# Kernel tuning notes

Hardware: AMD Instinct MI355X
Metric: run time of the kernel (lower is better)

Reference implementation:

```python
import jax, jax.numpy as jnp
import numpy as np

MAX_H = 64
MAX_W = 64

def setup_inputs() -> dict:
    key = jax.random.key(0)
    ks = jax.random.split(key, 6)
    in_f, out_f = 128, 128
    x0 = jax.random.normal(ks[0], (32, 64, 64, in_f), dtype=jnp.float32)
    x1 = jax.random.normal(ks[1], (32, 32, 64, in_f), dtype=jnp.float32)
    x2 = jax.random.normal(ks[2], (32, 64, 32, in_f), dtype=jnp.float32)
    x3 = jax.random.normal(ks[3], (32, 32, 32, in_f), dtype=jnp.float32)
    stdv = 1.0 / np.sqrt(in_f)
    weight = jax.random.uniform(ks[4], (out_f, in_f), minval=-stdv, maxval=stdv, dtype=jnp.float32)
    bias = jax.random.uniform(ks[5], (out_f,), minval=-stdv, maxval=stdv, dtype=jnp.float32)
    return {"x0": x0, "x1": x1, "x2": x2, "x3": x3, "weight": weight, "bias": bias}

def reference(x0, x1, x2, x3, weight, bias):
    # Grouped/ragged linear: flatten each variable-shaped tensor to rows of
    # in_features, concatenate, apply shared y = x @ W^T + b, then reshape to
    # (-1, max_H, max_W, out_features) as in the original CUDA path.
    k = weight.shape[0]
    flat = jnp.concatenate([x.reshape(-1, x.shape[-1]) for x in (x0, x1, x2, x3)], axis=0)
    out = flat @ weight.T + bias  # [total_rows, out_features]
    return out.reshape(-1, MAX_H, MAX_W, k)
```

## Files before the change

kernel.cpp:

```cpp
#include <hip/hip_runtime.h>
#include <hip/hip_bf16.h>


typedef __attribute__((ext_vector_type(8))) short bf8_t;
typedef __attribute__((ext_vector_type(4))) float f4_t;

__device__ __forceinline__ short bfc(float f) {
    return __builtin_bit_cast(short, __float2bfloat16(f));
}

__device__ __forceinline__ unsigned short f2bf_rne(float f) {
    unsigned u = __builtin_bit_cast(unsigned, f);
    u += 0x7fffu + ((u >> 16) & 1u);
    return (unsigned short)(u >> 16);
}

#define SEG0 131072L
#define SEG1 196608L
#define SEG2 262144L

__device__ __forceinline__ void resolve(long gr,
    const float* __restrict__ x0, const float* __restrict__ x1,
    const float* __restrict__ x2, const float* __restrict__ x3,
    float* __restrict__ out, const float** xr, float** orow)
{
    const float* xp; long loc;
    if      (gr < SEG0) { xp = x0; loc = gr; }
    else if (gr < SEG1) { xp = x1; loc = gr - SEG0; }
    else if (gr < SEG2) { xp = x2; loc = gr - SEG1; }
    else                { xp = x3; loc = gr - SEG2; }
    *xr   = xp + loc * 128;
    *orow = out + gr * 128;
}

__device__ __forceinline__ void load_tile(f4_t (&raw)[8], const float* __restrict__ rowbase, int lk)
{
#pragma unroll
    for (int ks = 0; ks < 4; ++ks) {
        const float* p = rowbase + ks * 32 + lk * 8;
        raw[2 * ks]     = *reinterpret_cast<const f4_t*>(p);
        raw[2 * ks + 1] = *reinterpret_cast<const f4_t*>(p + 4);
    }
}

__device__ __forceinline__ void compute_store(
    const f4_t (&raw)[8], const unsigned short* __restrict__ Wl,
    const float* __restrict__ bl, float* __restrict__ orow,
    int lm, int lk, int nsw)
{
    bf8_t xf[4];
#pragma unroll
    for (int ks = 0; ks < 4; ++ks) {
        bf8_t t;
        t[0] = bfc(raw[2 * ks].x);
        t[1] = bfc(raw[2 * ks].y);
        t[2] = bfc(raw[2 * ks].z);
        t[3] = bfc(raw[2 * ks].w);
        t[4] = bfc(raw[2 * ks + 1].x);
        t[5] = bfc(raw[2 * ks + 1].y);
        t[6] = bfc(raw[2 * ks + 1].z);
        t[7] = bfc(raw[2 * ks + 1].w);
        xf[ks] = t;
    }

    f4_t acc[8];
#pragma unroll
    for (int nt = 0; nt < 8; ++nt)
        acc[nt] = *reinterpret_cast<const f4_t*>(&bl[nt * 16 + lk * 4]);

#pragma unroll
    for (int nt = 0; nt < 8; ++nt) {
        const int nrow = nt * 16 + lm;
#pragma unroll
        for (int ks = 0; ks < 4; ++ks) {
            const int c = (ks * 4 + lk) ^ nsw;
            bf8_t wf = *reinterpret_cast<const bf8_t*>(&Wl[nrow * 128 + c * 8]);
            acc[nt] = __builtin_amdgcn_mfma_f32_16x16x32_bf16(wf, xf[ks], acc[nt], 0, 0, 0);
        }
    }

#pragma unroll
    for (int nt = 0; nt < 8; ++nt)
        __builtin_nontemporal_store(acc[nt], reinterpret_cast<f4_t*>(orow + nt * 16 + lk * 4));
}

__global__ __launch_bounds__(256)
void lin_kernel(const float* __restrict__ x0, const float* __restrict__ x1,
                const float* __restrict__ x2, const float* __restrict__ x3,
                const float* __restrict__ W, const float* __restrict__ bias,
                float* __restrict__ out)
{
    __shared__ unsigned short Wl[128 * 128];
    __shared__ float bl[128];

    const int tid = threadIdx.x;

#pragma unroll
    for (int i = 0; i < 16; ++i) {
        int f  = i * 256 + tid;
        int n  = f >> 5;
        int k4 = f & 31;
        f4_t v = reinterpret_cast<const f4_t*>(W)[f];
        unsigned long long p =
              (unsigned long long)f2bf_rne(v.x)
            | ((unsigned long long)f2bf_rne(v.y) << 16)
            | ((unsigned long long)f2bf_rne(v.z) << 32)
            | ((unsigned long long)f2bf_rne(v.w) << 48);
        int sc = (k4 >> 1) ^ (n & 7);
        *reinterpret_cast<unsigned long long*>(&Wl[n * 128 + sc * 8 + (k4 & 1) * 4]) = p;
    }
    if (tid < 128) bl[tid] = bias[tid];
    __syncthreads();

    const int wave = tid >> 6;
    const int lane = tid & 63;
    const int lm   = lane & 15;
    const int lk   = lane >> 4;
    const int nsw  = lm & 7;

    const long r0 = (long)blockIdx.x * 384 + wave * 96 + lm;

    f4_t rawA[8], rawB[8];
    const float* xA; const float* xB;
    float* oA; float* oB;

    resolve(r0 +  0, x0, x1, x2, x3, out, &xA, &oA); load_tile(rawA, xA, lk);
    resolve(r0 + 16, x0, x1, x2, x3, out, &xB, &oB); load_tile(rawB, xB, lk);
    compute_store(rawA, Wl, bl, oA, lm, lk, nsw);
    resolve(r0 + 32, x0, x1, x2, x3, out, &xA, &oA); load_tile(rawA, xA, lk);
    compute_store(rawB, Wl, bl, oB, lm, lk, nsw);
    resolve(r0 + 48, x0, x1, x2, x3, out, &xB, &oB); load_tile(rawB, xB, lk);
    compute_store(rawA, Wl, bl, oA, lm, lk, nsw);
    resolve(r0 + 64, x0, x1, x2, x3, out, &xA, &oA); load_tile(rawA, xA, lk);
    compute_store(rawB, Wl, bl, oB, lm, lk, nsw);
    resolve(r0 + 80, x0, x1, x2, x3, out, &xB, &oB); load_tile(rawB, xB, lk);
    compute_store(rawA, Wl, bl, oA, lm, lk, nsw);
    compute_store(rawB, Wl, bl, oB, lm, lk, nsw);
}

extern "C" void kernel_launch(void* const* d_in, const int* in_sizes, int n_in,
                              void* d_out, int out_size, void* d_ws, size_t ws_size,
                              hipStream_t stream) {
    const float* x0 = (const float*)d_in[0];
    const float* x1 = (const float*)d_in[1];
    const float* x2 = (const float*)d_in[2];
    const float* x3 = (const float*)d_in[3];
    const float* W  = (const float*)d_in[4];
    const float* b  = (const float*)d_in[5];
    float* out = (float*)d_out;

    hipLaunchKernelGGL(lin_kernel, dim3(768), dim3(256), 0, stream,
                       x0, x1, x2, x3, W, b, out);
}
```

Measured before the change: 61.76 us.

## Switch to 32x32x16 bf16 MFMA with 32-row tiles and interleaved row mapping

Replaces the 16x16x32 MFMA tiles with 32x32x16 MFMA, so each wave handles 32-row tiles and 4 output-column tiles with 16-wide accumulators. Rows are reassigned so the four waves interleave within 128-row strides, and each block now processes three row tiles per wave instead of six. The output stores change from nontemporal to ordinary vector stores. The aim is fewer MFMA and LDS weight-read instructions per output. In exchange, register pressure rises (16-float raw buffers, wider accumulators), and per-lane stores and loads each cover only 32 bytes, which may hurt coalescing.

After: 74.44 us. +20.5%, slower.

```diff
diff --git a/kernel.cpp b/kernel.cpp
--- a/kernel.cpp
+++ b/kernel.cpp
@@ -2,8 +2,9 @@
 #include <hip/hip_bf16.h>
 
 
-typedef __attribute__((ext_vector_type(8))) short bf8_t;
-typedef __attribute__((ext_vector_type(4))) float f4_t;
+typedef __attribute__((ext_vector_type(8)))  short bf8_t;
+typedef __attribute__((ext_vector_type(4)))  float f4_t;
+typedef __attribute__((ext_vector_type(16))) float f16_t;
 
 __device__ __forceinline__ short bfc(float f) {
     return __builtin_bit_cast(short, __float2bfloat16(f));
@@ -33,55 +34,61 @@
     *orow = out + gr * 128;
 }
 
-__device__ __forceinline__ void load_tile(f4_t (&raw)[8], const float* __restrict__ rowbase, int lk)
+__device__ __forceinline__ void load_tile(f4_t (&raw)[16], const float* __restrict__ xrow, int hi)
 {
 #pragma unroll
-    for (int ks = 0; ks < 4; ++ks) {
-        const float* p = rowbase + ks * 32 + lk * 8;
+    for (int ks = 0; ks < 8; ++ks) {
+        const float* p = xrow + ks * 16 + hi * 8;
         raw[2 * ks]     = *reinterpret_cast<const f4_t*>(p);
         raw[2 * ks + 1] = *reinterpret_cast<const f4_t*>(p + 4);
     }
 }
 
 __device__ __forceinline__ void compute_store(
-    const f4_t (&raw)[8], const unsigned short* __restrict__ Wl,
+    const f4_t (&raw)[16], const unsigned short* __restrict__ Wl,
     const float* __restrict__ bl, float* __restrict__ orow,
-    int lm, int lk, int nsw)
+    int xm, int hi, int nsw)
 {
-    bf8_t xf[4];
+    f16_t acc[4];
 #pragma unroll
-    for (int ks = 0; ks < 4; ++ks) {
-        bf8_t t;
-        t[0] = bfc(raw[2 * ks].x);
-        t[1] = bfc(raw[2 * ks].y);
-        t[2] = bfc(raw[2 * ks].z);
-        t[3] = bfc(raw[2 * ks].w);
-        t[4] = bfc(raw[2 * ks + 1].x);
-        t[5] = bfc(raw[2 * ks + 1].y);
-        t[6] = bfc(raw[2 * ks + 1].z);
-        t[7] = bfc(raw[2 * ks + 1].w);
-        xf[ks] = t;
-    }
-
-    f4_t acc[8];
+    for (int nt = 0; nt < 4; ++nt) {
 #pragma unroll
-    for (int nt = 0; nt < 8; ++nt)
-        acc[nt] = *reinterpret_cast<const f4_t*>(&bl[nt * 16 + lk * 4]);
-
-#pragma unroll
-    for (int nt = 0; nt < 8; ++nt) {
-        const int nrow = nt * 16 + lm;
-#pragma unroll
-        for (int ks = 0; ks < 4; ++ks) {
-            const int c = (ks * 4 + lk) ^ nsw;
-            bf8_t wf = *reinterpret_cast<const bf8_t*>(&Wl[nrow * 128 + c * 8]);
-            acc[nt] = __builtin_amdgcn_mfma_f32_16x16x32_bf16(wf, xf[ks], acc[nt], 0, 0, 0);
+        for (int q = 0; q < 4; ++q) {
+            f4_t b4 = *reinterpret_cast<const f4_t*>(&bl[nt * 32 + q * 8 + hi * 4]);
+            acc[nt][4 * q + 0] = b4.x;
+            acc[nt][4 * q + 1] = b4.y;
+            acc[nt][4 * q + 2] = b4.z;
+            acc[nt][4 * q + 3] = b4.w;
         }
     }
 
 #pragma unroll
-    for (int nt = 0; nt < 8; ++nt)
-        __builtin_nontemporal_store(acc[nt], reinterpret_cast<f4_t*>(orow + nt * 16 + lk * 4));
+    for (int ks = 0; ks < 8; ++ks) {
+        f4_t a = raw[2 * ks], b = raw[2 * ks + 1];
+        bf8_t xf;
+        xf[0] = bfc(a.x); xf[1] = bfc(a.y); xf[2] = bfc(a.z); xf[3] = bfc(a.w);
+        xf[4] = bfc(b.x); xf[5] = bfc(b.y); xf[6] = bfc(b.z); xf[7] = bfc(b.w);
+        const int c = ((2 * ks + hi) ^ nsw) * 8;
+#pragma unroll
+        for (int nt = 0; nt < 4; ++nt) {
+            const int nrow = nt * 32 + xm;
+            bf8_t wf = *reinterpret_cast<const bf8_t*>(&Wl[nrow * 128 + c]);
+            acc[nt] = __builtin_amdgcn_mfma_f32_32x32x16_bf16(wf, xf, acc[nt], 0, 0, 0);
+        }
+    }
+
+#pragma unroll
+    for (int nt = 0; nt < 4; ++nt) {
+#pragma unroll
+        for (int q = 0; q < 4; ++q) {
+            f4_t v;
+            v.x = acc[nt][4 * q + 0];
+            v.y = acc[nt][4 * q + 1];
+            v.z = acc[nt][4 * q + 2];
+            v.w = acc[nt][4 * q + 3];
+            *reinterpret_cast<f4_t*>(orow + nt * 32 + q * 8 + hi * 4) = v;
+        }
+    }
 }
 
 __global__ __launch_bounds__(256)
@@ -114,28 +121,22 @@
 
     const int wave = tid >> 6;
     const int lane = tid & 63;
-    const int lm   = lane & 15;
-    const int lk   = lane >> 4;
-    const int nsw  = lm & 7;
+    const int xm   = lane & 31;
+    const int hi   = lane >> 5;
+    const int nsw  = lane & 7;
 
-    const long r0 = (long)blockIdx.x * 384 + wave * 96 + lm;
+    const long r0 = (long)blockIdx.x * 384 + wave * 32 + xm;
 
-    f4_t rawA[8], rawB[8];
+    f4_t rawA[16], rawB[16];
     const float* xA; const float* xB;
     float* oA; float* oB;
 
-    resolve(r0 +  0, x0, x1, x2, x3, out, &xA, &oA); load_tile(rawA, xA, lk);
-    resolve(r0 + 16, x0, x1, x2, x3, out, &xB, &oB); load_tile(rawB, xB, lk);
-    compute_store(rawA, Wl, bl, oA, lm, lk, nsw);
-    resolve(r0 + 32, x0, x1, x2, x3, out, &xA, &oA); load_tile(rawA, xA, lk);
-    compute_store(rawB, Wl, bl, oB, lm, lk, nsw);
-    resolve(r0 + 48, x0, x1, x2, x3, out, &xB, &oB); load_tile(rawB, xB, lk);
-    compute_store(rawA, Wl, bl, oA, lm, lk, nsw);
-    resolve(r0 + 64, x0, x1, x2, x3, out, &xA, &oA); load_tile(rawA, xA, lk);
-    compute_store(rawB, Wl, bl, oB, lm, lk, nsw);
-    resolve(r0 + 80, x0, x1, x2, x3, out, &xB, &oB); load_tile(rawB, xB, lk);
-    compute_store(rawA, Wl, bl, oA, lm, lk, nsw);
-    compute_store(rawB, Wl, bl, oB, lm, lk, nsw);
+    resolve(r0 +   0, x0, x1, x2, x3, out, &xA, &oA); load_tile(rawA, xA, hi);
+    resolve(r0 + 128, x0, x1, x2, x3, out, &xB, &oB); load_tile(rawB, xB, hi);
+    compute_store(rawA, Wl, bl, oA, xm, hi, nsw);
+    resolve(r0 + 256, x0, x1, x2, x3, out, &xA, &oA); load_tile(rawA, xA, hi);
+    compute_store(rawB, Wl, bl, oB, xm, hi, nsw);
+    compute_store(rawA, Wl, bl, oA, xm, hi, nsw);
 }
 
 extern "C" void kernel_launch(void* const* d_in, const int* in_sizes, int n_in,
```

## Rebalance row tiles across 1024 blocks with interleaved wave tiles and regular stores

Applied to the files above, without the earlier changes.

The grid grows from 768 to 1024 blocks of 288 rows each. Waves interleave 16-row tiles, with waves 0-1 taking 5 tiles and waves 2-3 taking 4, in a double-buffered runtime loop. Nontemporal output stores are replaced with ordinary stores. The aim is to fill all CUs more evenly; the cost is that each block repeats the W conversion into LDS, and the dynamic loop may add register or scheduling overhead.

Result: slower. 64.75 us (+4.8%).

```diff
diff --git a/kernel.cpp b/kernel.cpp
--- a/kernel.cpp
+++ b/kernel.cpp
@@ -51,15 +51,10 @@
     bf8_t xf[4];
 #pragma unroll
     for (int ks = 0; ks < 4; ++ks) {
+        f4_t a = raw[2 * ks], b = raw[2 * ks + 1];
         bf8_t t;
-        t[0] = bfc(raw[2 * ks].x);
-        t[1] = bfc(raw[2 * ks].y);
-        t[2] = bfc(raw[2 * ks].z);
-        t[3] = bfc(raw[2 * ks].w);
-        t[4] = bfc(raw[2 * ks + 1].x);
-        t[5] = bfc(raw[2 * ks + 1].y);
-        t[6] = bfc(raw[2 * ks + 1].z);
-        t[7] = bfc(raw[2 * ks + 1].w);
+        t[0]=bfc(a.x); t[1]=bfc(a.y); t[2]=bfc(a.z); t[3]=bfc(a.w);
+        t[4]=bfc(b.x); t[5]=bfc(b.y); t[6]=bfc(b.z); t[7]=bfc(b.w);
         xf[ks] = t;
     }
 
@@ -81,7 +76,7 @@
 
 #pragma unroll
     for (int nt = 0; nt < 8; ++nt)
-        __builtin_nontemporal_store(acc[nt], reinterpret_cast<f4_t*>(orow + nt * 16 + lk * 4));
+        *reinterpret_cast<f4_t*>(orow + nt * 16 + lk * 4) = acc[nt];
 }
 
 __global__ __launch_bounds__(256)
@@ -118,24 +113,32 @@
     const int lk   = lane >> 4;
     const int nsw  = lm & 7;
 
-    const long r0 = (long)blockIdx.x * 384 + wave * 96 + lm;
+    const long blk0  = (long)blockIdx.x * 288;
+    const int  ntile = (wave < 2) ? 5 : 4;
 
     f4_t rawA[8], rawB[8];
     const float* xA; const float* xB;
     float* oA; float* oB;
 
-    resolve(r0 +  0, x0, x1, x2, x3, out, &xA, &oA); load_tile(rawA, xA, lk);
-    resolve(r0 + 16, x0, x1, x2, x3, out, &xB, &oB); load_tile(rawB, xB, lk);
-    compute_store(rawA, Wl, bl, oA, lm, lk, nsw);
-    resolve(r0 + 32, x0, x1, x2, x3, out, &xA, &oA); load_tile(rawA, xA, lk);
-    compute_store(rawB, Wl, bl, oB, lm, lk, nsw);
-    resolve(r0 + 48, x0, x1, x2, x3, out, &xB, &oB); load_tile(rawB, xB, lk);
-    compute_store(rawA, Wl, bl, oA, lm, lk, nsw);
-    resolve(r0 + 64, x0, x1, x2, x3, out, &xA, &oA); load_tile(rawA, xA, lk);
-    compute_store(rawB, Wl, bl, oB, lm, lk, nsw);
-    resolve(r0 + 80, x0, x1, x2, x3, out, &xB, &oB); load_tile(rawB, xB, lk);
-    compute_store(rawA, Wl, bl, oA, lm, lk, nsw);
-    compute_store(rawB, Wl, bl, oB, lm, lk, nsw);
+    resolve(blk0 + (long)(wave * 16) + lm, x0, x1, x2, x3, out, &xA, &oA);
+    load_tile(rawA, xA, lk);
+
+    int j = 0;
+    while (true) {
+        if (j + 1 < ntile) {
+            resolve(blk0 + (long)((wave + 4 * (j + 1)) * 16) + lm, x0, x1, x2, x3, out, &xB, &oB);
+            load_tile(rawB, xB, lk);
+        }
+        compute_store(rawA, Wl, bl, oA, lm, lk, nsw);
+        if (++j == ntile) break;
+
+        if (j + 1 < ntile) {
+            resolve(blk0 + (long)((wave + 4 * (j + 1)) * 16) + lm, x0, x1, x2, x3, out, &xA, &oA);
+            load_tile(rawA, xA, lk);
+        }
+        compute_store(rawB, Wl, bl, oB, lm, lk, nsw);
+        if (++j == ntile) break;
+    }
 }
 
 extern "C" void kernel_launch(void* const* d_in, const int* in_sizes, int n_in,
@@ -149,6 +152,6 @@
     const float* b  = (const float*)d_in[5];
     float* out = (float*)d_out;
 
-    hipLaunchKernelGGL(lin_kernel, dim3(768), dim3(256), 0, stream,
+    hipLaunchKernelGGL(lin_kernel, dim3(1024), dim3(256), 0, stream,
                        x0, x1, x2, x3, W, b, out);
 }
```
